# Performance work log

Hardware: AMD Instinct MI355X
Metric: run time of the kernel (lower is better)

The kernel has to match this reference:

```python
import jax, jax.numpy as jnp
import numpy as np

B, L, H = 2, 2048, 2048
NH, KVH = 16, 4
D = H // NH          # 128
G = NH // KVH        # 4 query heads per kv head
LN_EPS = 1e-12


def setup_inputs() -> dict:
    key = jax.random.key(0)
    ks = jax.random.split(key, 6)
    s = 0.02
    return {
        "hidden_state": jax.random.normal(ks[0], (B, L, H), jnp.float32),
        "mask": jnp.zeros((B, 1, 1, L), jnp.float32),
        "Wq": jax.random.normal(ks[1], (H, H), jnp.float32) * s,
        "bq": jnp.zeros((H,), jnp.float32),
        "Wk": jax.random.normal(ks[2], (KVH * D, H), jnp.float32) * s,
        "bk": jnp.zeros((KVH * D,), jnp.float32),
        "Wv": jax.random.normal(ks[3], (KVH * D, H), jnp.float32) * s,
        "bv": jnp.zeros((KVH * D,), jnp.float32),
        "Wo": jax.random.normal(ks[4], (H, H), jnp.float32) * s,
        "bo": jnp.zeros((H,), jnp.float32),
        "ln_g": jnp.ones((H,), jnp.float32),
        "ln_b": jnp.zeros((H,), jnp.float32),
    }


def _layernorm(x, g, b):
    mu = jnp.mean(x, axis=-1, keepdims=True)
    var = jnp.mean(jnp.square(x - mu), axis=-1, keepdims=True)
    return (x - mu) * jax.lax.rsqrt(var + LN_EPS) * g + b


def reference(hidden_state, mask, Wq, bq, Wk, bk, Wv, bv, Wo, bo, ln_g, ln_b):
    x = hidden_state
    # projections: b l (h d)
    q = x @ Wq.T + bq            # [B,L,NH*D]
    k = x @ Wk.T + bk            # [B,L,KVH*D]
    v = x @ Wv.T + bv            # [B,L,KVH*D]
    # b l (h d) -> b h l d, with q heads grouped per kv head (GQA broadcast,
    # mathematically identical to repeat_kv + dense SDPA)
    q = q.reshape(B, L, KVH, G, D).transpose(0, 2, 3, 1, 4)   # [B,KVH,G,L,D]
    k = k.reshape(B, L, KVH, D).transpose(0, 2, 1, 3)         # [B,KVH,L,D]
    v = v.reshape(B, L, KVH, D).transpose(0, 2, 1, 3)         # [B,KVH,L,D]
    scale = 1.0 / jnp.sqrt(jnp.float32(D))
    scores = jnp.einsum('bkgld,bkmd->bkglm', q, k) * scale    # [B,KVH,G,L,L]
    scores = scores + mask[:, :, None]                         # broadcast [B,1,1,1,L]
    attn = jax.nn.softmax(scores, axis=-1)
    out = jnp.einsum('bkglm,bkmd->bkgld', attn, v)            # [B,KVH,G,L,D]
    out = out.transpose(0, 3, 1, 2, 4).reshape(B, L, H)       # b h l d -> b l (h d)
    # SelfOutput: dense + residual + layernorm
    out = out @ Wo.T + bo
    return _layernorm(out + x, ln_g, ln_b)
```

## Files before the change

### kernel.cpp

```cpp
#include <hip/hip_runtime.h>
#include <math.h>

typedef short v8s __attribute__((ext_vector_type(8)));
typedef float v4f __attribute__((ext_vector_type(4)));
typedef unsigned long long ull;

constexpr int L_ = 2048;
constexpr int H_ = 2048;
constexpr float LOG2E = 1.4426950408889634f;
constexpr float QSCALE = 0.08838834764831845f * LOG2E;

__device__ inline unsigned short f2bf(float f) {
    unsigned int u = __float_as_uint(f);
    u += 0x7fffu + ((u >> 16) & 1u);
    return (unsigned short)(u >> 16);
}

__device__ inline void async16(const void* g, void* l) {
    __builtin_amdgcn_global_load_lds(
        (const __attribute__((address_space(1))) unsigned int*)g,
        (__attribute__((address_space(3))) unsigned int*)l, 16, 0, 0);
}

__global__ __launch_bounds__(256) void conv_all(
    const float* __restrict__ x,  const float* __restrict__ wq,
    const float* __restrict__ wk, const float* __restrict__ wv,
    const float* __restrict__ wo, const float* __restrict__ mask,
    unsigned short* __restrict__ xb, unsigned short* __restrict__ wqkvb,
    unsigned short* __restrict__ wob, float* __restrict__ maskL)
{
    int u = blockIdx.x * 256 + threadIdx.x;
    const float* s;
    unsigned short* d;
    if (u < 1048576)      { s = x  + (size_t)u * 8;             d = xb   + (size_t)u * 8; }
    else if (u < 1572864) { size_t t = (size_t)(u - 1048576) * 8; s = wq + t; d = wqkvb + t; }
    else if (u < 1703936) { size_t t = (size_t)(u - 1572864) * 8; s = wk + t; d = wqkvb + (size_t)2048 * 2048 + t; }
    else if (u < 1835008) { size_t t = (size_t)(u - 1703936) * 8; s = wv + t; d = wqkvb + (size_t)2560 * 2048 + t; }
    else if (u < 2359296) { size_t t = (size_t)(u - 1835008) * 8; s = wo + t; d = wob + t; }
    else if (u < 2359808) {
        int m = (u - 2359296) * 8;
        float4 a = *(const float4*)(mask + m);
        float4 b = *(const float4*)(mask + m + 4);
        float4 oa = {a.x * LOG2E, a.y * LOG2E, a.z * LOG2E, a.w * LOG2E};
        float4 ob = {b.x * LOG2E, b.y * LOG2E, b.z * LOG2E, b.w * LOG2E};
        *(float4*)(maskL + m) = oa;
        *(float4*)(maskL + m + 4) = ob;
        return;
    } else return;
    float4 a = *(const float4*)s;
    float4 b = *(const float4*)(s + 4);
    v8s o;
    o[0] = (short)f2bf(a.x); o[1] = (short)f2bf(a.y);
    o[2] = (short)f2bf(a.z); o[3] = (short)f2bf(a.w);
    o[4] = (short)f2bf(b.x); o[5] = (short)f2bf(b.y);
    o[6] = (short)f2bf(b.z); o[7] = (short)f2bf(b.w);
    *(v8s*)d = o;
}

template <int MODE>
__global__ __launch_bounds__(256) void gemm_mfma(
    const unsigned short* __restrict__ A, const unsigned short* __restrict__ W,
    const float* __restrict__ b0, const float* __restrict__ b1,
    const float* __restrict__ b2,
    unsigned short* __restrict__ oq, unsigned short* __restrict__ ok,
    unsigned short* __restrict__ ov,
    float* __restrict__ of, const float* __restrict__ resid,
    int K, int N)
{
    __shared__ short SM[3 * 8192];

    const int tid  = threadIdx.x;
    const int lane = tid & 63;
    const int wave = tid >> 6;
    const int lid  = lane & 15;
    const int g    = lane >> 4;
    const int wr   = wave >> 1, wc = wave & 1;
    const int row0 = blockIdx.y * 128, col0 = blockIdx.x * 128;

    auto stage = [&](int k0, int buf) {
#pragma unroll
        for (int i = 0; i < 2; ++i) {
            int idx = tid + i * 256;
            int r = idx >> 2, s = idx & 3;
            int c = s ^ ((r >> 1) & 3);
            async16(A + (size_t)(row0 + r) * K + k0 + c * 8,
                    &SM[buf * 8192 + idx * 8]);
            async16(W + (size_t)(col0 + r) * K + k0 + c * 8,
                    &SM[buf * 8192 + 4096 + idx * 8]);
        }
    };

    v4f acc[4][4];
#pragma unroll
    for (int i = 0; i < 4; ++i)
#pragma unroll
        for (int j = 0; j < 4; ++j) acc[i][j] = (v4f){0.f, 0.f, 0.f, 0.f};

    stage(0, 0);
    stage(32, 1);
    int p = 0;
    for (int k0 = 0; k0 < K; k0 += 32) {
        __syncthreads();
        if (k0 + 64 < K) {
            int nb = p + 2; if (nb >= 3) nb -= 3;
            stage(k0 + 64, nb);
        }
        const short* As = &SM[p * 8192];
        const short* Bs = &SM[p * 8192 + 4096];

        v8s af[4], bf[4];
#pragma unroll
        for (int t = 0; t < 4; ++t) {
            int ra = wr * 64 + t * 16 + lid;
            int rb = wc * 64 + t * 16 + lid;
            af[t] = *(const v8s*)&As[ra * 32 + ((g ^ ((ra >> 1) & 3)) * 8)];
            bf[t] = *(const v8s*)&Bs[rb * 32 + ((g ^ ((rb >> 1) & 3)) * 8)];
        }
#pragma unroll
        for (int mt = 0; mt < 4; ++mt)
#pragma unroll
            for (int nt = 0; nt < 4; ++nt)
                acc[mt][nt] = __builtin_amdgcn_mfma_f32_16x16x32_bf16(
                    af[mt], bf[nt], acc[mt][nt], 0, 0, 0);
        if (++p == 3) p = 0;
    }

    const int crow = row0 + wr * 64, ccol = col0 + wc * 64;
    if (MODE == 0) {
#pragma unroll
        for (int mt = 0; mt < 4; ++mt)
#pragma unroll
            for (int nt = 0; nt < 4; ++nt) {
                int cc = ccol + nt * 16 + lid;
                float bb = b0[cc];
#pragma unroll
                for (int r = 0; r < 4; ++r) {
                    int rr = crow + mt * 16 + g * 4 + r;
                    of[(size_t)rr * N + cc] =
                        acc[mt][nt][r] + bb + resid[(size_t)rr * N + cc];
                }
            }
    } else {
        const int seg = (col0 < 2048) ? 0 : (col0 < 2560 ? 1 : 2);
#pragma unroll
        for (int mt = 0; mt < 4; ++mt)
#pragma unroll
            for (int nt = 0; nt < 4; ++nt) {
                int cc = ccol + nt * 16 + lid;
                if (seg == 0) {
                    float bb = b0[cc];
#pragma unroll
                    for (int r = 0; r < 4; ++r) {
                        int rr = crow + mt * 16 + g * 4 + r;
                        oq[(size_t)rr * 2048 + cc] =
                            f2bf((acc[mt][nt][r] + bb) * QSCALE);
                    }
                } else if (seg == 1) {
                    float bb = b1[cc - 2048];
#pragma unroll
                    for (int r = 0; r < 4; ++r) {
                        int rr = crow + mt * 16 + g * 4 + r;
                        ok[(size_t)rr * 512 + (cc - 2048)] =
                            f2bf(acc[mt][nt][r] + bb);
                    }
                } else {
                    float bb = b2[cc - 2560];
#pragma unroll
                    for (int r = 0; r < 4; ++r) {
                        int rr = crow + mt * 16 + g * 4 + r;
                        ov[(size_t)rr * 512 + (cc - 2560)] =
                            f2bf(acc[mt][nt][r] + bb);
                    }
                }
            }
    }
}

__global__ __launch_bounds__(256) void transpose_v(
    const unsigned short* __restrict__ V, unsigned short* __restrict__ Vt)
{
    __shared__ unsigned short T[64][72];
    const int r0 = blockIdx.y * 64;
    const int c0 = blockIdx.x * 64;
    const int tid = threadIdx.x;
    const int r = tid >> 3, c8 = (tid & 7) * 8;
#pragma unroll
    for (int h = 0; h < 2; ++h) {
        v8s val = *(const v8s*)&V[(size_t)(r0 + h * 32 + r) * 512 + c0 + c8];
#pragma unroll
        for (int e = 0; e < 8; ++e) T[c8 + e][h * 32 + r] = (unsigned short)val[e];
    }
    __syncthreads();
#pragma unroll
    for (int h = 0; h < 2; ++h) {
        int idx = tid + h * 256;
        int ci = idx >> 3, ch = (idx & 7) * 8;
        v8s o = *(const v8s*)&T[ci][ch];
        int rr = r0 + ch;
        *(v8s*)&Vt[((size_t)((rr >> 11) * 512 + c0 + ci)) * 2048 + (rr & 2047)] = o;
    }
}

__global__ __launch_bounds__(256) void flash_mfma(
    const unsigned short* __restrict__ Q,
    const unsigned short* __restrict__ K,
    const unsigned short* __restrict__ Vt,
    const float* __restrict__ maskL,
    unsigned short* __restrict__ AO)
{
    __shared__ short K_s[2][32 * 128];
    __shared__ short V_s[2][128 * 32];
    __shared__ short P_s[64 * 32];

    const int tid  = threadIdx.x;
    const int lane = tid & 63;
    const int wave = tid >> 6;
    const int lid  = lane & 15;
    const int g    = lane >> 4;
    const int h    = blockIdx.y;
    const int b    = blockIdx.z;
    const int kvh  = h >> 2;
    const int q0   = blockIdx.x * 64;
    const int wq   = wave * 16;

    auto stage = [&](int k0, int buf) {
#pragma unroll
        for (int i = 0; i < 2; ++i) {
            int idx = tid + i * 256;
            int kr = idx >> 4, ks = idx & 15;
            async16(K + ((size_t)(b * L_ + k0 + kr)) * 512 + kvh * 128 +
                        ((ks ^ (kr & 15)) * 8),
                    &K_s[buf][idx * 8]);
            int vd = idx >> 2, vs = idx & 3;
            async16(Vt + ((size_t)(b * 512 + kvh * 128 + vd)) * 2048 + k0 +
                         ((vs ^ (vd & 3)) * 8),
                    &V_s[buf][idx * 8]);
        }
    };

    v8s bq[4];
    {
        const size_t base = ((size_t)(b * L_ + q0 + wq + lid)) * 2048 + h * 128;
#pragma unroll
        for (int kc = 0; kc < 4; ++kc)
            bq[kc] = *(const v8s*)(Q + base + kc * 32 + g * 8);
    }

    v4f oacc[8];
#pragma unroll
    for (int nt = 0; nt < 8; ++nt) oacc[nt] = (v4f){0.f, 0.f, 0.f, 0.f};
    float lsm = 0.f;

    stage(0, 0);
    for (int it = 0; it < 64; ++it) {
        const int p = it & 1;
        const int k0 = it * 32;
        __syncthreads();
        if (it + 1 < 64) stage(k0 + 32, p ^ 1);

        v4f sacc[2];
        sacc[0] = (v4f){0.f, 0.f, 0.f, 0.f};
        sacc[1] = (v4f){0.f, 0.f, 0.f, 0.f};
#pragma unroll
        for (int kc = 0; kc < 4; ++kc)
#pragma unroll
            for (int kt = 0; kt < 2; ++kt) {
                v8s ak = *(const v8s*)&K_s[p][(kt * 16 + lid) * 128 +
                                              (((kc * 4 + g) ^ lid) * 8)];
                sacc[kt] = __builtin_amdgcn_mfma_f32_16x16x32_bf16(
                    ak, bq[kc], sacc[kt], 0, 0, 0);
            }

#pragma unroll
        for (int kt = 0; kt < 2; ++kt) {
            float4 mk = *(const float4*)&maskL[b * L_ + k0 + kt * 16 + g * 4];
            float m4[4] = {mk.x, mk.y, mk.z, mk.w};
#pragma unroll
            for (int r = 0; r < 4; ++r) {
                float e = __builtin_amdgcn_exp2f(sacc[kt][r] + m4[r]);
                sacc[kt][r] = e;
                lsm += e;
            }
        }

#pragma unroll
        for (int kt = 0; kt < 2; ++kt) {
            ull pk = (ull)f2bf(sacc[kt][0]) |
                     ((ull)f2bf(sacc[kt][1]) << 16) |
                     ((ull)f2bf(sacc[kt][2]) << 32) |
                     ((ull)f2bf(sacc[kt][3]) << 48);
            int slot = (kt * 2 + (g >> 1)) ^ (lid & 3);
            *(ull*)&P_s[(wq + lid) * 32 + slot * 8 + (g & 1) * 4] = pk;
        }

        v8s ap = *(const v8s*)&P_s[(wq + lid) * 32 + ((g ^ (lid & 3)) * 8)];
#pragma unroll
        for (int nt = 0; nt < 8; ++nt) {
            v8s bv = *(const v8s*)&V_s[p][(nt * 16 + lid) * 32 +
                                          ((g ^ (lid & 3)) * 8)];
            oacc[nt] = __builtin_amdgcn_mfma_f32_16x16x32_bf16(
                ap, bv, oacc[nt], 0, 0, 0);
        }
    }

    lsm += __shfl_xor(lsm, 16);
    lsm += __shfl_xor(lsm, 32);
    float linv[4];
#pragma unroll
    for (int r = 0; r < 4; ++r) linv[r] = 1.0f / __shfl(lsm, g * 4 + r);
#pragma unroll
    for (int nt = 0; nt < 8; ++nt)
#pragma unroll
        for (int r = 0; r < 4; ++r) {
            size_t orow = (size_t)(b * L_ + q0 + wq + g * 4 + r);
            AO[orow * 2048 + h * 128 + nt * 16 + lid] =
                f2bf(oacc[nt][r] * linv[r]);
        }
}

__global__ __launch_bounds__(256) void ln_kernel(
    const float* __restrict__ P, const float* __restrict__ g,
    const float* __restrict__ bta, float* __restrict__ Out)
{
    const int row = blockIdx.x;
    const int tid = threadIdx.x;
    const float* p = P + (size_t)row * H_;

    float vals[8];
    float s = 0.f;
#pragma unroll
    for (int it = 0; it < 2; ++it) {
        int c = tid * 4 + it * 1024;
        float4 a = *(const float4*)&p[c];
        vals[it * 4 + 0] = a.x; vals[it * 4 + 1] = a.y;
        vals[it * 4 + 2] = a.z; vals[it * 4 + 3] = a.w;
        s += a.x + a.y + a.z + a.w;
    }
    __shared__ float red[4];
    float t = s;
#pragma unroll
    for (int off = 32; off > 0; off >>= 1) t += __shfl_xor(t, off);
    if ((tid & 63) == 0) red[tid >> 6] = t;
    __syncthreads();
    float mean = (red[0] + red[1] + red[2] + red[3]) * (1.f / (float)H_);

    float vsum = 0.f;
#pragma unroll
    for (int i = 0; i < 8; ++i) {
        float d = vals[i] - mean;
        vsum += d * d;
    }
    __syncthreads();
    t = vsum;
#pragma unroll
    for (int off = 32; off > 0; off >>= 1) t += __shfl_xor(t, off);
    if ((tid & 63) == 0) red[tid >> 6] = t;
    __syncthreads();
    float var = (red[0] + red[1] + red[2] + red[3]) * (1.f / (float)H_);
    float rs  = 1.f / sqrtf(var + 1e-12f);

#pragma unroll
    for (int it = 0; it < 2; ++it) {
        int c = tid * 4 + it * 1024;
        float4 gv = *(const float4*)&g[c];
        float4 bv = *(const float4*)&bta[c];
        float4 ov;
        ov.x = (vals[it * 4 + 0] - mean) * rs * gv.x + bv.x;
        ov.y = (vals[it * 4 + 1] - mean) * rs * gv.y + bv.y;
        ov.z = (vals[it * 4 + 2] - mean) * rs * gv.z + bv.z;
        ov.w = (vals[it * 4 + 3] - mean) * rs * gv.w + bv.w;
        *(float4*)&Out[(size_t)row * H_ + c] = ov;
    }
}

extern "C" void kernel_launch(void* const* d_in, const int* in_sizes, int n_in,
                              void* d_out, int out_size, void* d_ws, size_t ws_size,
                              hipStream_t stream)
{
    const float* x    = (const float*)d_in[0];
    const float* mask = (const float*)d_in[1];
    const float* Wq   = (const float*)d_in[2];
    const float* bq   = (const float*)d_in[3];
    const float* Wk   = (const float*)d_in[4];
    const float* bk   = (const float*)d_in[5];
    const float* Wv   = (const float*)d_in[6];
    const float* bv   = (const float*)d_in[7];
    const float* Wo   = (const float*)d_in[8];
    const float* bo   = (const float*)d_in[9];
    const float* lng  = (const float*)d_in[10];
    const float* lnb  = (const float*)d_in[11];
    float* out = (float*)d_out;

    char* ws = (char*)d_ws;
    unsigned short* xb    = (unsigned short*)(ws);
    unsigned short* wqkv  = (unsigned short*)(ws + 16777216);
    float*          maskL = (float*)         (ws + 29360128);
    unsigned short* q     = (unsigned short*)(ws + 29376512);
    unsigned short* k     = (unsigned short*)(ws + 46153728);
    unsigned short* vnat  = (unsigned short*)(ws + 50348032);
    unsigned short* vt    = (unsigned short*)(ws + 54542336);
    unsigned short* ao    = (unsigned short*)(ws + 58736640);
    unsigned short* wob   = (unsigned short*)(ws + 75513856);
    float*          pj    = (float*)(ws);

    dim3 blk(256);
    conv_all<<<9218, blk, 0, stream>>>(x, Wq, Wk, Wv, Wo, mask,
                                       xb, wqkv, wob, maskL);

    gemm_mfma<3><<<dim3(24, 32), blk, 0, stream>>>(
        xb, wqkv, bq, bk, bv, q, k, vnat, nullptr, nullptr, 2048, 3072);

    transpose_v<<<dim3(8, 64), blk, 0, stream>>>(vnat, vt);

    flash_mfma<<<dim3(32, 16, 2), blk, 0, stream>>>(q, k, vt, maskL, ao);

    gemm_mfma<0><<<dim3(16, 32), blk, 0, stream>>>(
        ao, wob, bo, nullptr, nullptr, nullptr, nullptr, nullptr, pj, x, 2048, 2048);
    ln_kernel<<<4096, blk, 0, stream>>>(pj, lng, lnb, out);
}
```

Measured before the change: 374.9 us.

## Enlarge flash attention tile to 256 query rows with 8 waves

The flash attention kernel now runs 512 threads per block over 256 query rows, with each wave owning two 16-row query tiles. Each K and V fragment read from LDS is reused across both tiles, and the staging of K and V per iteration is amortized over four times as many queries. It also seeds the score accumulators with the mask, packs bf16 pairs with a perm instruction using round-half-up instead of round-to-nearest-even, and changes the V swizzle. The costs are higher register pressure and only 256 blocks in the grid, which may not fill all compute units.

```diff
diff --git a/kernel.cpp b/kernel.cpp
--- a/kernel.cpp
+++ b/kernel.cpp
@@ -14,6 +14,12 @@
     unsigned int u = __float_as_uint(f);
     u += 0x7fffu + ((u >> 16) & 1u);
     return (unsigned short)(u >> 16);
+}
+
+__device__ inline unsigned int pk2bf(float lo, float hi) {
+    unsigned int a = __float_as_uint(lo) + 0x8000u;
+    unsigned int b = __float_as_uint(hi) + 0x8000u;
+    return __builtin_amdgcn_perm(b, a, 0x07060302);
 }
 
 __device__ inline void async16(const void* g, void* l) {
@@ -201,7 +207,7 @@
     }
 }
 
-__global__ __launch_bounds__(256) void flash_mfma(
+__global__ __launch_bounds__(512) void flash_mfma(
     const unsigned short* __restrict__ Q,
     const unsigned short* __restrict__ K,
     const unsigned short* __restrict__ Vt,
@@ -210,112 +216,140 @@
 {
     __shared__ short K_s[2][32 * 128];
     __shared__ short V_s[2][128 * 32];
-    __shared__ short P_s[64 * 32];
+    __shared__ short P_s[256 * 32];
 
     const int tid  = threadIdx.x;
     const int lane = tid & 63;
     const int wave = tid >> 6;
     const int lid  = lane & 15;
     const int g    = lane >> 4;
+    const int lh   = (lid >> 2) & 3;
     const int h    = blockIdx.y;
     const int b    = blockIdx.z;
     const int kvh  = h >> 2;
-    const int q0   = blockIdx.x * 64;
-    const int wq   = wave * 16;
-
-    auto stage = [&](int k0, int buf) {
-#pragma unroll
-        for (int i = 0; i < 2; ++i) {
-            int idx = tid + i * 256;
-            int kr = idx >> 4, ks = idx & 15;
-            async16(K + ((size_t)(b * L_ + k0 + kr)) * 512 + kvh * 128 +
-                        ((ks ^ (kr & 15)) * 8),
-                    &K_s[buf][idx * 8]);
-            int vd = idx >> 2, vs = idx & 3;
-            async16(Vt + ((size_t)(b * 512 + kvh * 128 + vd)) * 2048 + k0 +
-                         ((vs ^ (vd & 3)) * 8),
-                    &V_s[buf][idx * 8]);
-        }
-    };
-
-    v8s bq[4];
+    const int q0   = blockIdx.x * 256;
+    const int wq   = wave * 32;
+
+    const unsigned short* pK;
+    const unsigned short* pV;
+    {
+        int kr = tid >> 4, ks = tid & 15;
+        pK = K + ((size_t)(b * L_ + kr)) * 512 + kvh * 128 +
+             ((ks ^ (kr & 15)) * 8);
+        int vd = tid >> 2, vs = tid & 3;
+        pV = Vt + ((size_t)(b * 512 + kvh * 128 + vd)) * 2048 +
+             ((vs ^ ((vd >> 2) & 3)) * 8);
+    }
+    short* ldsK0 = &K_s[0][tid * 8];
+    short* ldsK1 = &K_s[1][tid * 8];
+    short* ldsV0 = &V_s[0][tid * 8];
+    short* ldsV1 = &V_s[1][tid * 8];
+
+    v8s bq[2][4];
     {
         const size_t base = ((size_t)(b * L_ + q0 + wq + lid)) * 2048 + h * 128;
 #pragma unroll
-        for (int kc = 0; kc < 4; ++kc)
-            bq[kc] = *(const v8s*)(Q + base + kc * 32 + g * 8);
-    }
-
-    v4f oacc[8];
-#pragma unroll
-    for (int nt = 0; nt < 8; ++nt) oacc[nt] = (v4f){0.f, 0.f, 0.f, 0.f};
-    float lsm = 0.f;
-
-    stage(0, 0);
+        for (int qt = 0; qt < 2; ++qt)
+#pragma unroll
+            for (int kc = 0; kc < 4; ++kc)
+                bq[qt][kc] = *(const v8s*)(Q + base + (size_t)qt * 16 * 2048 +
+                                           kc * 32 + g * 8);
+    }
+
+    v4f oacc[2][8];
+#pragma unroll
+    for (int mt = 0; mt < 2; ++mt)
+#pragma unroll
+        for (int nt = 0; nt < 8; ++nt) oacc[mt][nt] = (v4f){0.f, 0.f, 0.f, 0.f};
+    float lsm[2] = {0.f, 0.f};
+
+    async16(pK, ldsK0);
+    async16(pV, ldsV0);
+
     for (int it = 0; it < 64; ++it) {
         const int p = it & 1;
         const int k0 = it * 32;
         __syncthreads();
-        if (it + 1 < 64) stage(k0 + 32, p ^ 1);
-
-        v4f sacc[2];
-        sacc[0] = (v4f){0.f, 0.f, 0.f, 0.f};
-        sacc[1] = (v4f){0.f, 0.f, 0.f, 0.f};
-#pragma unroll
-        for (int kc = 0; kc < 4; ++kc)
-#pragma unroll
-            for (int kt = 0; kt < 2; ++kt) {
-                v8s ak = *(const v8s*)&K_s[p][(kt * 16 + lid) * 128 +
-                                              (((kc * 4 + g) ^ lid) * 8)];
-                sacc[kt] = __builtin_amdgcn_mfma_f32_16x16x32_bf16(
-                    ak, bq[kc], sacc[kt], 0, 0, 0);
-            }
-
+        pK += 32 * 512;
+        pV += 32;
+        if (it + 1 < 64) {
+            async16(pK, p ? ldsK0 : ldsK1);
+            async16(pV, p ? ldsV0 : ldsV1);
+        }
+        const short* Ks = K_s[p];
+        const short* Vs = V_s[p];
+
+        v4f sacc[2][2];
 #pragma unroll
         for (int kt = 0; kt < 2; ++kt) {
             float4 mk = *(const float4*)&maskL[b * L_ + k0 + kt * 16 + g * 4];
-            float m4[4] = {mk.x, mk.y, mk.z, mk.w};
+            v4f seed = {mk.x, mk.y, mk.z, mk.w};
+            sacc[kt][0] = seed;
+            sacc[kt][1] = seed;
+        }
+#pragma unroll
+        for (int kc = 0; kc < 4; ++kc)
+#pragma unroll
+            for (int kt = 0; kt < 2; ++kt) {
+                v8s ak = *(const v8s*)&Ks[(kt * 16 + lid) * 128 +
+                                          (((kc * 4 + g) ^ lid) * 8)];
+#pragma unroll
+                for (int qt = 0; qt < 2; ++qt)
+                    sacc[kt][qt] = __builtin_amdgcn_mfma_f32_16x16x32_bf16(
+                        ak, bq[qt][kc], sacc[kt][qt], 0, 0, 0);
+            }
+
+#pragma unroll
+        for (int kt = 0; kt < 2; ++kt)
+#pragma unroll
+            for (int qt = 0; qt < 2; ++qt) {
+                float e0 = __builtin_amdgcn_exp2f(sacc[kt][qt][0]);
+                float e1 = __builtin_amdgcn_exp2f(sacc[kt][qt][1]);
+                float e2 = __builtin_amdgcn_exp2f(sacc[kt][qt][2]);
+                float e3 = __builtin_amdgcn_exp2f(sacc[kt][qt][3]);
+                lsm[qt] += (e0 + e1) + (e2 + e3);
+                uint2 pk;
+                pk.x = pk2bf(e0, e1);
+                pk.y = pk2bf(e2, e3);
+                int qrow = wq + qt * 16 + lid;
+                int slot = (kt * 2 + (g >> 1)) ^ lh;
+                *(uint2*)&P_s[qrow * 32 + slot * 8 + (g & 1) * 4] = pk;
+            }
+
+        v8s ap[2];
+#pragma unroll
+        for (int mt = 0; mt < 2; ++mt)
+            ap[mt] = *(const v8s*)&P_s[(wq + mt * 16 + lid) * 32 +
+                                       ((g ^ lh) * 8)];
+#pragma unroll
+        for (int nt = 0; nt < 8; ++nt) {
+            v8s bv = *(const v8s*)&Vs[(nt * 16 + lid) * 32 + ((g ^ lh) * 8)];
+#pragma unroll
+            for (int mt = 0; mt < 2; ++mt)
+                oacc[mt][nt] = __builtin_amdgcn_mfma_f32_16x16x32_bf16(
+                    ap[mt], bv, oacc[mt][nt], 0, 0, 0);
+        }
+    }
+
+#pragma unroll
+    for (int qt = 0; qt < 2; ++qt) {
+        lsm[qt] += __shfl_xor(lsm[qt], 16);
+        lsm[qt] += __shfl_xor(lsm[qt], 32);
+    }
+#pragma unroll
+    for (int mt = 0; mt < 2; ++mt) {
+        float linv[4];
+#pragma unroll
+        for (int r = 0; r < 4; ++r) linv[r] = 1.0f / __shfl(lsm[mt], g * 4 + r);
+#pragma unroll
+        for (int nt = 0; nt < 8; ++nt)
 #pragma unroll
             for (int r = 0; r < 4; ++r) {
-                float e = __builtin_amdgcn_exp2f(sacc[kt][r] + m4[r]);
-                sacc[kt][r] = e;
-                lsm += e;
+                size_t orow = (size_t)(b * L_ + q0 + wq + mt * 16 + g * 4 + r);
+                AO[orow * 2048 + h * 128 + nt * 16 + lid] =
+                    f2bf(oacc[mt][nt][r] * linv[r]);
             }
-        }
-
-#pragma unroll
-        for (int kt = 0; kt < 2; ++kt) {
-            ull pk = (ull)f2bf(sacc[kt][0]) |
-                     ((ull)f2bf(sacc[kt][1]) << 16) |
-                     ((ull)f2bf(sacc[kt][2]) << 32) |
-                     ((ull)f2bf(sacc[kt][3]) << 48);
-            int slot = (kt * 2 + (g >> 1)) ^ (lid & 3);
-            *(ull*)&P_s[(wq + lid) * 32 + slot * 8 + (g & 1) * 4] = pk;
-        }
-
-        v8s ap = *(const v8s*)&P_s[(wq + lid) * 32 + ((g ^ (lid & 3)) * 8)];
-#pragma unroll
-        for (int nt = 0; nt < 8; ++nt) {
-            v8s bv = *(const v8s*)&V_s[p][(nt * 16 + lid) * 32 +
-                                          ((g ^ (lid & 3)) * 8)];
-            oacc[nt] = __builtin_amdgcn_mfma_f32_16x16x32_bf16(
-                ap, bv, oacc[nt], 0, 0, 0);
-        }
-    }
-
-    lsm += __shfl_xor(lsm, 16);
-    lsm += __shfl_xor(lsm, 32);
-    float linv[4];
-#pragma unroll
-    for (int r = 0; r < 4; ++r) linv[r] = 1.0f / __shfl(lsm, g * 4 + r);
-#pragma unroll
-    for (int nt = 0; nt < 8; ++nt)
-#pragma unroll
-        for (int r = 0; r < 4; ++r) {
-            size_t orow = (size_t)(b * L_ + q0 + wq + g * 4 + r);
-            AO[orow * 2048 + h * 128 + nt * 16 + lid] =
-                f2bf(oacc[nt][r] * linv[r]);
-        }
+    }
 }
 
 __global__ __launch_bounds__(256) void ln_kernel(
@@ -412,7 +446,7 @@
 
     transpose_v<<<dim3(8, 64), blk, 0, stream>>>(vnat, vt);
 
-    flash_mfma<<<dim3(32, 16, 2), blk, 0, stream>>>(q, k, vt, maskL, ao);
+    flash_mfma<<<dim3(8, 16, 2), dim3(512), 0, stream>>>(q, k, vt, maskL, ao);
 
     gemm_mfma<0><<<dim3(16, 32), blk, 0, stream>>>(
         ao, wob, bo, nullptr, nullptr, nullptr, nullptr, nullptr, pj, x, 2048, 2048);
```

New measurement: 347.7 us. 1.08x faster.
